# Optimization experiments

Hardware: AMD Instinct MI355X
Metric: run time of the kernel (lower is better)

## Reference

```python
import jax, jax.numpy as jnp
import numpy as np

B, S, H = 128, 512, 512

def _xavier(key, shape):
    fan_in, fan_out = shape[1], shape[0]
    limit = float(np.sqrt(6.0 / (fan_in + fan_out)))
    return jax.random.uniform(key, shape, jnp.float32, -limit, limit)

def setup_inputs() -> dict:
    key = jax.random.key(0)
    k1, k2, k3, k4, k5 = jax.random.split(key, 5)
    return {
        "h": jax.random.normal(k1, (B, S, H), jnp.float32),
        "x": jax.random.normal(k2, (B, S, H), jnp.float32),
        "Ve": _xavier(k3, (1, H)),
        "U1": _xavier(k4, (H, 2 * H)),
        "U2": _xavier(k5, (H, H)),
    }

def reference(h, x, Ve, U1, U2):
    # h: [B,S,H], x: [B,S,H]
    h_last = h[:, -1, :]                      # [B,H]
    U1a, U1b = U1[:, :U1.shape[0]], U1[:, U1.shape[0]:]  # each [H,H]
    # u1 = concat(h_t, h_last) @ U1.T, vectorized over t
    u1 = jnp.einsum('bsh,kh->bsk', h, U1a) + jnp.einsum('bh,kh->bk', h_last, U1b)[:, None, :]
    u2 = jnp.einsum('bsh,kh->bsk', x, U2)
    u = jnp.tanh(u1 + u2)                     # [B,S,H]
    e = jnp.einsum('bsk,k->bs', u, Ve[0])     # [B,S]
    alpha = jax.nn.softmax(e, axis=1)         # [B,S]
    context = jnp.einsum('bs,bsh->bh', alpha, h)
    return context
```

## Files before the change

kernel.cpp:

```cpp
#include <hip/hip_runtime.h>
#include <cstdint>
#include <cstddef>


typedef _Float16 h8 __attribute__((ext_vector_type(8)));
typedef float    f4 __attribute__((ext_vector_type(4)));

#define GLOAD16(g, l)                                                          \
  __builtin_amdgcn_global_load_lds(                                            \
      (const __attribute__((address_space(1))) void*)(g),                      \
      (__attribute__((address_space(3))) void*)(l), 16, 0, 0)

__device__ __forceinline__ float fast_tanh(float v) {
  float ex = __expf(2.0f * v);
  return 1.0f - 2.0f / (ex + 1.0f);
}

__global__ __launch_bounds__(256)
void cvt_kernel(const float* __restrict__ src, _Float16* __restrict__ dst, int n8) {
  const int stride = gridDim.x * 256;
  for (int i = blockIdx.x * 256 + threadIdx.x; i < n8; i += stride) {
    const float* p = src + (size_t)i * 8;
    f4 a = *(const f4*)p, b = *(const f4*)(p + 4);
    _Float16 hv[8];
    hv[0]=(_Float16)a[0]; hv[1]=(_Float16)a[1]; hv[2]=(_Float16)a[2]; hv[3]=(_Float16)a[3];
    hv[4]=(_Float16)b[0]; hv[5]=(_Float16)b[1]; hv[6]=(_Float16)b[2]; hv[7]=(_Float16)b[3];
    *(uint4*)(dst + (size_t)i * 8) = *(uint4*)hv;
  }
}

__global__ void bsetup2_kernel(const float* __restrict__ U1, const float* __restrict__ U2,
                               _Float16* __restrict__ Bimg) {
  int g = blockIdx.x * 256 + threadIdx.x;
  int l15 = g & 15;
  int grp = (g >> 4) & 7;
  int s   = (g >> 7) & 7;
  int kt  = (g >> 10) & 15;
  int nt  = g >> 14;
  int n = nt * 128 + grp * 16 + l15;
  int k = kt * 64 + s * 8;
  const float* p = (k < 512) ? (U1 + (size_t)n * 1024 + k)
                             : (U2 + (size_t)n * 512 + (k - 512));
  f4 a = *(const f4*)p, b = *(const f4*)(p + 4);
  _Float16 hv[8];
  hv[0]=(_Float16)a[0]; hv[1]=(_Float16)a[1]; hv[2]=(_Float16)a[2]; hv[3]=(_Float16)a[3];
  hv[4]=(_Float16)b[0]; hv[5]=(_Float16)b[1]; hv[6]=(_Float16)b[2]; hv[7]=(_Float16)b[3];
  *(uint4*)(Bimg + (size_t)g * 8) = *(uint4*)hv;
}

__global__ void bias_kernel(const float* __restrict__ hT, const float* __restrict__ U1,
                            float* __restrict__ bias) {
  const int b = blockIdx.x, t = threadIdx.x;
  const int l = t & 63, w = t >> 6;
  __shared__ float4 hl[128];
  if (t < 128) hl[t] = *(const float4*)(hT + ((size_t)b * 512 + 511) * 512 + t * 4);
  __syncthreads();
  for (int n = w; n < 512; n += 4) {
    const float4* ur = (const float4*)(U1 + (size_t)n * 1024 + 512);
    float4 u0 = ur[l],      u1 = ur[l + 64];
    float4 h0 = hl[l],      h1 = hl[l + 64];
    float s = u0.x*h0.x + u0.y*h0.y + u0.z*h0.z + u0.w*h0.w
            + u1.x*h1.x + u1.y*h1.y + u1.z*h1.z + u1.w*h1.w;
#pragma unroll
    for (int d = 1; d < 64; d <<= 1) s += __shfl_xor(s, d, 64);
    if (l == 0) bias[(size_t)b * 512 + n] = s;
  }
}

__global__ __launch_bounds__(256, 2)
void gemm3_kernel(const _Float16* __restrict__ hF, const _Float16* __restrict__ xF,
                  const _Float16* __restrict__ Bimg, const float* __restrict__ bias,
                  const float* __restrict__ Ve, float* __restrict__ e) {
  const int bid  = ((int)blockIdx.x & 7) * 256 + ((int)blockIdx.x >> 3);
  const int bm   = bid >> 2;
  const int nt   = bid & 3;
  const int row0 = bm * 128;
  const int bb   = row0 >> 9;
  const int t    = threadIdx.x;
  const int l    = t & 63;
  const int wv   = t >> 6;
  const int wm   = wv >> 1, wn = wv & 1;
  const int l15  = l & 15, lhi = l >> 4;

  __shared__ __align__(16) _Float16 Asm[2][8192];
  __shared__ __align__(16) _Float16 Bsm[2][8192];

  const int aoff0 = (wv * 32 + (l >> 3)) * 512 + (((l & 7) ^ (l >> 3)) << 3);

  auto STAGE = [&](int c, int kt) {
    const _Float16* ah = ((kt < 8) ? hF : xF) + (size_t)row0 * 512 + (kt & 7) * 64;
#pragma unroll
    for (int j = 0; j < 4; ++j)
      GLOAD16(ah + aoff0 + j * 4096, &Asm[c][wv * 2048 + j * 512]);
    const _Float16* bt = Bimg + ((size_t)(nt * 16 + kt) << 13);
#pragma unroll
    for (int j = 0; j < 4; ++j)
      GLOAD16(bt + wv * 2048 + j * 512 + l * 8, &Bsm[c][wv * 2048 + j * 512]);
  };

  const int vA0 = wm * 4096 + l15 * 64 + (((0 + lhi) ^ (l15 & 7)) << 3);
  const int vA1 = wm * 4096 + l15 * 64 + (((4 + lhi) ^ (l15 & 7)) << 3);
  const int vB  = lhi * 1024 + wn * 512 + l15 * 8;

  f4 acc[4][4];
#pragma unroll
  for (int mf = 0; mf < 4; ++mf)
#pragma unroll
    for (int nf = 0; nf < 4; ++nf)
      acc[mf][nf] = (f4){0.f, 0.f, 0.f, 0.f};

  STAGE(0, 0);
  STAGE(1, 1);
  asm volatile("s_waitcnt vmcnt(8)\n\ts_barrier" ::: "memory");
  __builtin_amdgcn_sched_barrier(0);

  for (int kt = 0; kt < 16; ++kt) {
    const int c = kt & 1;
#pragma unroll
    for (int kk = 0; kk < 2; ++kk) {
      h8 af[4], bf[4];
      const int a0 = (kk ? vA1 : vA0);
#pragma unroll
      for (int mf = 0; mf < 4; ++mf)
        af[mf] = *(const h8*)&Asm[c][a0 + mf * 1024];
#pragma unroll
      for (int nf = 0; nf < 4; ++nf)
        bf[nf] = *(const h8*)&Bsm[c][vB + kk * 4096 + nf * 128];
#pragma unroll
      for (int mf = 0; mf < 4; ++mf)
#pragma unroll
        for (int nf = 0; nf < 4; ++nf)
          acc[mf][nf] = __builtin_amdgcn_mfma_f32_16x16x32_f16(af[mf], bf[nf], acc[mf][nf], 0, 0, 0);
    }
    if (kt == 15) break;
    asm volatile("s_waitcnt lgkmcnt(0)\n\ts_barrier" ::: "memory");
    __builtin_amdgcn_sched_barrier(0);
    if (kt < 14) {
      STAGE(c, kt + 2);
      asm volatile("s_waitcnt vmcnt(8)\n\ts_barrier" ::: "memory");
    } else {
      asm volatile("s_waitcnt vmcnt(0)\n\ts_barrier" ::: "memory");
    }
    __builtin_amdgcn_sched_barrier(0);
  }

  float vev[4], biasv[4];
#pragma unroll
  for (int nf = 0; nf < 4; ++nf) {
    int c = nt * 128 + wn * 64 + nf * 16 + l15;
    vev[nf]   = Ve[c];
    biasv[nf] = bias[(size_t)bb * 512 + c];
  }
#pragma unroll
  for (int mf = 0; mf < 4; ++mf) {
#pragma unroll
    for (int j = 0; j < 4; ++j) {
      float s = 0.f;
#pragma unroll
      for (int nf = 0; nf < 4; ++nf)
        s += fast_tanh(acc[mf][nf][j] + biasv[nf]) * vev[nf];
#pragma unroll
      for (int m = 1; m < 16; m <<= 1) s += __shfl_xor(s, m, 64);
      if (l15 == 0) atomicAdd(&e[row0 + wm * 64 + mf * 16 + lhi * 4 + j], s);
    }
  }
}

__global__ __launch_bounds__(512)
void smax_ctx_kernel(const _Float16* __restrict__ hF, const float* __restrict__ e,
                     float* __restrict__ out) {
  const int b  = blockIdx.x >> 2;
  const int sc = blockIdx.x & 3;
  const int t  = threadIdx.x;
  __shared__ float al[512];
  __shared__ float redm[8], reds[8];
  float v = e[(size_t)b * 512 + t];
  float m = v;
#pragma unroll
  for (int d = 1; d < 64; d <<= 1) m = fmaxf(m, __shfl_xor(m, d, 64));
  if ((t & 63) == 0) redm[t >> 6] = m;
  __syncthreads();
  m = redm[0];
#pragma unroll
  for (int i = 1; i < 8; ++i) m = fmaxf(m, redm[i]);
  float ev = __expf(v - m);
  al[t] = ev;
  float s = ev;
#pragma unroll
  for (int d = 1; d < 64; d <<= 1) s += __shfl_xor(s, d, 64);
  if ((t & 63) == 0) reds[t >> 6] = s;
  __syncthreads();
  s = reds[0];
#pragma unroll
  for (int i = 1; i < 8; ++i) s += reds[i];
  const float inv = 1.0f / s;
  const _Float16* hp = hF + ((size_t)b * 512 + sc * 128) * 512 + t;
  float acc = 0.f;
#pragma unroll 4
  for (int q = 0; q < 128; ++q) acc += al[sc * 128 + q] * (float)hp[(size_t)q * 512];
  atomicAdd(&out[(size_t)b * 512 + t], acc * inv);
}

extern "C" void kernel_launch(void* const* d_in, const int* in_sizes, int n_in,
                              void* d_out, int out_size, void* d_ws, size_t ws_size,
                              hipStream_t stream) {
  const float* h  = (const float*)d_in[0];
  const float* x  = (const float*)d_in[1];
  const float* Ve = (const float*)d_in[2];
  const float* U1 = (const float*)d_in[3];
  const float* U2 = (const float*)d_in[4];
  float* out = (float*)d_out;

  const size_t MB = 1u << 20;
  if (ws_size < 130 * MB) return;

  _Float16* hF   = (_Float16*)d_ws;
  _Float16* xF   = (_Float16*)((char*)d_ws + 64 * MB);
  _Float16* Bimg = (_Float16*)((char*)d_ws + 128 * MB);
  float*    bias = (float*)((char*)d_ws + 129 * MB);
  float*    e    = (float*)((char*)d_ws + 129 * MB + 256 * 1024);

  hipMemsetAsync(e, 0, 65536 * sizeof(float), stream);
  hipMemsetAsync(d_out, 0, 65536 * sizeof(float), stream);

  cvt_kernel<<<4096, 256, 0, stream>>>(h, hF, 4194304);
  cvt_kernel<<<4096, 256, 0, stream>>>(x, xF, 4194304);
  bsetup2_kernel<<<256, 256, 0, stream>>>(U1, U2, Bimg);
  bias_kernel<<<128, 256, 0, stream>>>(h, U1, bias);
  gemm3_kernel<<<2048, 256, 0, stream>>>(hF, xF, Bimg, bias, Ve, e);
  smax_ctx_kernel<<<512, 512, 0, stream>>>(hF, e, out);
}
```

Measured before the change: 275.6 us.

## Use 8-wave GEMM blocks with smaller per-wave tiles and merge conversion kernels

The GEMM block grows from 4 to 8 waves (512 threads), and each wave now computes a 64x32 tile instead of 64x64, which halves its accumulator registers and raises occupancy. The B-operand image layout is changed to match the new wave split. The pipeline moves from a hand-tuned two-stage prefetch with explicit vmcnt waits to a simpler prefetch-next-stage scheme using __syncthreads. The two h/x fp16 conversion launches are merged into one kernel. The trade-off is less per-wave operand reuse and coarser synchronization, in exchange for more waves available to hide latency.

Measured after the change: 290.2 us. +5.3%, slower.

```diff
diff --git a/kernel.cpp b/kernel.cpp
--- a/kernel.cpp
+++ b/kernel.cpp
@@ -17,28 +17,33 @@
 }
 
 __global__ __launch_bounds__(256)
-void cvt_kernel(const float* __restrict__ src, _Float16* __restrict__ dst, int n8) {
+void cvt2_kernel(const float* __restrict__ h, const float* __restrict__ x,
+                 _Float16* __restrict__ hF, _Float16* __restrict__ xF) {
   const int stride = gridDim.x * 256;
-  for (int i = blockIdx.x * 256 + threadIdx.x; i < n8; i += stride) {
-    const float* p = src + (size_t)i * 8;
+  for (int i = blockIdx.x * 256 + threadIdx.x; i < 8388608; i += stride) {
+    const bool isH = i < 4194304;
+    const float* p = (isH ? h : x) + ((size_t)(i & 4194303)) * 8;
+    _Float16* d = (isH ? hF : xF) + ((size_t)(i & 4194303)) * 8;
     f4 a = *(const f4*)p, b = *(const f4*)(p + 4);
     _Float16 hv[8];
     hv[0]=(_Float16)a[0]; hv[1]=(_Float16)a[1]; hv[2]=(_Float16)a[2]; hv[3]=(_Float16)a[3];
     hv[4]=(_Float16)b[0]; hv[5]=(_Float16)b[1]; hv[6]=(_Float16)b[2]; hv[7]=(_Float16)b[3];
-    *(uint4*)(dst + (size_t)i * 8) = *(uint4*)hv;
-  }
-}
-
-__global__ void bsetup2_kernel(const float* __restrict__ U1, const float* __restrict__ U2,
+    *(uint4*)d = *(uint4*)hv;
+  }
+}
+
+__global__ void bsetup3_kernel(const float* __restrict__ U1, const float* __restrict__ U2,
                                _Float16* __restrict__ Bimg) {
   int g = blockIdx.x * 256 + threadIdx.x;
-  int l15 = g & 15;
-  int grp = (g >> 4) & 7;
-  int s   = (g >> 7) & 7;
+  int gt  = g & 1023;
   int kt  = (g >> 10) & 15;
   int nt  = g >> 14;
-  int n = nt * 128 + grp * 16 + l15;
-  int k = kt * 64 + s * 8;
+  int l15 = gt & 15;
+  int nf  = (gt >> 4) & 1;
+  int wn  = (gt >> 5) & 3;
+  int c8  = gt >> 7;
+  int n = nt * 128 + wn * 32 + nf * 16 + l15;
+  int k = kt * 64 + c8 * 8;
   const float* p = (k < 512) ? (U1 + (size_t)n * 1024 + k)
                              : (U2 + (size_t)n * 512 + (k - 512));
   f4 a = *(const f4*)p, b = *(const f4*)(p + 4);
@@ -67,8 +72,8 @@
   }
 }
 
-__global__ __launch_bounds__(256, 2)
-void gemm3_kernel(const _Float16* __restrict__ hF, const _Float16* __restrict__ xF,
+__global__ __launch_bounds__(512, 4)
+void gemm4_kernel(const _Float16* __restrict__ hF, const _Float16* __restrict__ xF,
                   const _Float16* __restrict__ Bimg, const float* __restrict__ bias,
                   const float* __restrict__ Ve, float* __restrict__ e) {
   const int bid  = ((int)blockIdx.x & 7) * 256 + ((int)blockIdx.x >> 3);
@@ -79,75 +84,63 @@
   const int t    = threadIdx.x;
   const int l    = t & 63;
   const int wv   = t >> 6;
-  const int wm   = wv >> 1, wn = wv & 1;
+  const int wm   = wv >> 2, wn = wv & 3;
   const int l15  = l & 15, lhi = l >> 4;
 
   __shared__ __align__(16) _Float16 Asm[2][8192];
   __shared__ __align__(16) _Float16 Bsm[2][8192];
 
-  const int aoff0 = (wv * 32 + (l >> 3)) * 512 + (((l & 7) ^ (l >> 3)) << 3);
+  const int aoff0 = (wv * 16 + (l >> 3)) * 512 + (((l & 7) ^ (l >> 3)) << 3);
 
   auto STAGE = [&](int c, int kt) {
     const _Float16* ah = ((kt < 8) ? hF : xF) + (size_t)row0 * 512 + (kt & 7) * 64;
-#pragma unroll
-    for (int j = 0; j < 4; ++j)
-      GLOAD16(ah + aoff0 + j * 4096, &Asm[c][wv * 2048 + j * 512]);
+    GLOAD16(ah + aoff0,        &Asm[c][wv * 1024]);
+    GLOAD16(ah + aoff0 + 4096, &Asm[c][wv * 1024 + 512]);
     const _Float16* bt = Bimg + ((size_t)(nt * 16 + kt) << 13);
-#pragma unroll
-    for (int j = 0; j < 4; ++j)
-      GLOAD16(bt + wv * 2048 + j * 512 + l * 8, &Bsm[c][wv * 2048 + j * 512]);
+    GLOAD16(bt + (wv * 128 + l) * 8,        &Bsm[c][wv * 1024]);
+    GLOAD16(bt + (wv * 128 + 64 + l) * 8,   &Bsm[c][wv * 1024 + 512]);
   };
 
-  const int vA0 = wm * 4096 + l15 * 64 + (((0 + lhi) ^ (l15 & 7)) << 3);
-  const int vA1 = wm * 4096 + l15 * 64 + (((4 + lhi) ^ (l15 & 7)) << 3);
-  const int vB  = lhi * 1024 + wn * 512 + l15 * 8;
-
-  f4 acc[4][4];
+  const int vA  = (wm * 64 + l15) * 64;
+  const int vB0 = wn * 256 + l15 * 8;
+
+  f4 acc[4][2];
 #pragma unroll
   for (int mf = 0; mf < 4; ++mf)
 #pragma unroll
-    for (int nf = 0; nf < 4; ++nf)
+    for (int nf = 0; nf < 2; ++nf)
       acc[mf][nf] = (f4){0.f, 0.f, 0.f, 0.f};
 
   STAGE(0, 0);
-  STAGE(1, 1);
-  asm volatile("s_waitcnt vmcnt(8)\n\ts_barrier" ::: "memory");
-  __builtin_amdgcn_sched_barrier(0);
+  __syncthreads();
 
   for (int kt = 0; kt < 16; ++kt) {
     const int c = kt & 1;
+    if (kt < 15) STAGE(c ^ 1, kt + 1);
 #pragma unroll
     for (int kk = 0; kk < 2; ++kk) {
-      h8 af[4], bf[4];
-      const int a0 = (kk ? vA1 : vA0);
+      const int c8 = kk * 4 + lhi;
+      const int aoffk = vA + ((c8 ^ (l15 & 7)) << 3);
+      h8 af[4], bf[2];
 #pragma unroll
       for (int mf = 0; mf < 4; ++mf)
-        af[mf] = *(const h8*)&Asm[c][a0 + mf * 1024];
-#pragma unroll
-      for (int nf = 0; nf < 4; ++nf)
-        bf[nf] = *(const h8*)&Bsm[c][vB + kk * 4096 + nf * 128];
+        af[mf] = *(const h8*)&Asm[c][aoffk + mf * 1024];
+#pragma unroll
+      for (int nf = 0; nf < 2; ++nf)
+        bf[nf] = *(const h8*)&Bsm[c][c8 * 1024 + vB0 + nf * 128];
 #pragma unroll
       for (int mf = 0; mf < 4; ++mf)
 #pragma unroll
-        for (int nf = 0; nf < 4; ++nf)
+        for (int nf = 0; nf < 2; ++nf)
           acc[mf][nf] = __builtin_amdgcn_mfma_f32_16x16x32_f16(af[mf], bf[nf], acc[mf][nf], 0, 0, 0);
     }
-    if (kt == 15) break;
-    asm volatile("s_waitcnt lgkmcnt(0)\n\ts_barrier" ::: "memory");
-    __builtin_amdgcn_sched_barrier(0);
-    if (kt < 14) {
-      STAGE(c, kt + 2);
-      asm volatile("s_waitcnt vmcnt(8)\n\ts_barrier" ::: "memory");
-    } else {
-      asm volatile("s_waitcnt vmcnt(0)\n\ts_barrier" ::: "memory");
-    }
-    __builtin_amdgcn_sched_barrier(0);
-  }
-
-  float vev[4], biasv[4];
-#pragma unroll
-  for (int nf = 0; nf < 4; ++nf) {
-    int c = nt * 128 + wn * 64 + nf * 16 + l15;
+    __syncthreads();
+  }
+
+  float vev[2], biasv[2];
+#pragma unroll
+  for (int nf = 0; nf < 2; ++nf) {
+    int c = nt * 128 + wn * 32 + nf * 16 + l15;
     vev[nf]   = Ve[c];
     biasv[nf] = bias[(size_t)bb * 512 + c];
   }
@@ -155,10 +148,8 @@
   for (int mf = 0; mf < 4; ++mf) {
 #pragma unroll
     for (int j = 0; j < 4; ++j) {
-      float s = 0.f;
-#pragma unroll
-      for (int nf = 0; nf < 4; ++nf)
-        s += fast_tanh(acc[mf][nf][j] + biasv[nf]) * vev[nf];
+      float s = fast_tanh(acc[mf][0][j] + biasv[0]) * vev[0]
+              + fast_tanh(acc[mf][1][j] + biasv[1]) * vev[1];
 #pragma unroll
       for (int m = 1; m < 16; m <<= 1) s += __shfl_xor(s, m, 64);
       if (l15 == 0) atomicAdd(&e[row0 + wm * 64 + mf * 16 + lhi * 4 + j], s);
@@ -223,10 +214,9 @@
   hipMemsetAsync(e, 0, 65536 * sizeof(float), stream);
   hipMemsetAsync(d_out, 0, 65536 * sizeof(float), stream);
 
-  cvt_kernel<<<4096, 256, 0, stream>>>(h, hF, 4194304);
-  cvt_kernel<<<4096, 256, 0, stream>>>(x, xF, 4194304);
-  bsetup2_kernel<<<256, 256, 0, stream>>>(U1, U2, Bimg);
+  cvt2_kernel<<<4096, 256, 0, stream>>>(h, x, hF, xF);
+  bsetup3_kernel<<<256, 256, 0, stream>>>(U1, U2, Bimg);
   bias_kernel<<<128, 256, 0, stream>>>(h, U1, bias);
-  gemm3_kernel<<<2048, 256, 0, stream>>>(hF, xF, Bimg, bias, Ve, e);
+  gemm4_kernel<<<2048, 512, 0, stream>>>(hF, xF, Bimg, bias, Ve, e);
   smax_ctx_kernel<<<512, 512, 0, stream>>>(hF, e, out);
 }
```

## Widen GEMM tile to 128x256 with 8 waves, triple-buffered LDS pipeline

Applied to the files above, without the earlier changes.

The GEMM now uses 512-thread blocks, each computing a 128x256 output tile. The pre-swizzled B image is re-laid out to match, so each block reads the A rows once per two column tiles instead of four. The LDS pipeline moves from double to triple buffering, with loads issued before compute so only one barrier is needed per k-step, and MFMA sections are raised in priority with s_setprio. The two conversion kernels are merged into one launch, and the bias kernel is reorganised so each wave keeps one U1 row in registers while looping over the batch. In exchange, the larger LDS footprint (144 KB per block) may limit occupancy.

Result: no change. 272.9 us (-1.0%).

```diff
diff --git a/kernel.cpp b/kernel.cpp
--- a/kernel.cpp
+++ b/kernel.cpp
@@ -17,28 +17,34 @@
 }
 
 __global__ __launch_bounds__(256)
-void cvt_kernel(const float* __restrict__ src, _Float16* __restrict__ dst, int n8) {
+void cvt2_kernel(const float* __restrict__ h, const float* __restrict__ x,
+                 _Float16* __restrict__ hF, _Float16* __restrict__ xF) {
   const int stride = gridDim.x * 256;
-  for (int i = blockIdx.x * 256 + threadIdx.x; i < n8; i += stride) {
-    const float* p = src + (size_t)i * 8;
+  for (int i = blockIdx.x * 256 + threadIdx.x; i < 8388608; i += stride) {
+    const bool isH = i < 4194304;
+    const float* p = (isH ? h : x) + ((size_t)(i & 4194303)) * 8;
+    _Float16* d = (isH ? hF : xF) + ((size_t)(i & 4194303)) * 8;
     f4 a = *(const f4*)p, b = *(const f4*)(p + 4);
     _Float16 hv[8];
     hv[0]=(_Float16)a[0]; hv[1]=(_Float16)a[1]; hv[2]=(_Float16)a[2]; hv[3]=(_Float16)a[3];
     hv[4]=(_Float16)b[0]; hv[5]=(_Float16)b[1]; hv[6]=(_Float16)b[2]; hv[7]=(_Float16)b[3];
-    *(uint4*)(dst + (size_t)i * 8) = *(uint4*)hv;
-  }
-}
-
-__global__ void bsetup2_kernel(const float* __restrict__ U1, const float* __restrict__ U2,
+    *(uint4*)d = *(uint4*)hv;
+  }
+}
+
+__global__ void bsetup4_kernel(const float* __restrict__ U1, const float* __restrict__ U2,
                                _Float16* __restrict__ Bimg) {
   int g = blockIdx.x * 256 + threadIdx.x;
-  int l15 = g & 15;
-  int grp = (g >> 4) & 7;
-  int s   = (g >> 7) & 7;
-  int kt  = (g >> 10) & 15;
-  int nt  = g >> 14;
-  int n = nt * 128 + grp * 16 + l15;
-  int k = kt * 64 + s * 8;
+  int c   = g & 2047;
+  int kt  = (g >> 11) & 15;
+  int nt  = g >> 15;
+  int l15 = c & 15;
+  int lhi = (c >> 4) & 3;
+  int kk  = (c >> 6) & 1;
+  int nf  = (c >> 7) & 3;
+  int wn  = c >> 9;
+  int n = nt * 256 + wn * 64 + nf * 16 + l15;
+  int k = kt * 64 + kk * 32 + lhi * 8;
   const float* p = (k < 512) ? (U1 + (size_t)n * 1024 + k)
                              : (U2 + (size_t)n * 512 + (k - 512));
   f4 a = *(const f4*)p, b = *(const f4*)(p + 4);
@@ -48,17 +54,17 @@
   *(uint4*)(Bimg + (size_t)g * 8) = *(uint4*)hv;
 }
 
-__global__ void bias_kernel(const float* __restrict__ hT, const float* __restrict__ U1,
-                            float* __restrict__ bias) {
-  const int b = blockIdx.x, t = threadIdx.x;
-  const int l = t & 63, w = t >> 6;
-  __shared__ float4 hl[128];
-  if (t < 128) hl[t] = *(const float4*)(hT + ((size_t)b * 512 + 511) * 512 + t * 4);
-  __syncthreads();
-  for (int n = w; n < 512; n += 4) {
-    const float4* ur = (const float4*)(U1 + (size_t)n * 1024 + 512);
-    float4 u0 = ur[l],      u1 = ur[l + 64];
-    float4 h0 = hl[l],      h1 = hl[l + 64];
+__global__ __launch_bounds__(256)
+void bias2_kernel(const float* __restrict__ hT, const float* __restrict__ U1,
+                  float* __restrict__ bias) {
+  const int t = threadIdx.x, l = t & 63, w = t >> 6;
+  const int n = blockIdx.x * 4 + w;
+  const float4* ur = (const float4*)(U1 + (size_t)n * 1024 + 512);
+  const float4 u0 = ur[l], u1 = ur[l + 64];
+#pragma unroll 4
+  for (int b = 0; b < 128; ++b) {
+    const float4* hp = (const float4*)(hT + ((size_t)b * 512 + 511) * 512);
+    float4 h0 = hp[l], h1 = hp[l + 64];
     float s = u0.x*h0.x + u0.y*h0.y + u0.z*h0.z + u0.w*h0.w
             + u1.x*h1.x + u1.y*h1.y + u1.z*h1.z + u1.w*h1.w;
 #pragma unroll
@@ -67,40 +73,44 @@
   }
 }
 
-__global__ __launch_bounds__(256, 2)
-void gemm3_kernel(const _Float16* __restrict__ hF, const _Float16* __restrict__ xF,
+__global__ __launch_bounds__(512, 2)
+void gemm5_kernel(const _Float16* __restrict__ hF, const _Float16* __restrict__ xF,
                   const _Float16* __restrict__ Bimg, const float* __restrict__ bias,
                   const float* __restrict__ Ve, float* __restrict__ e) {
-  const int bid  = ((int)blockIdx.x & 7) * 256 + ((int)blockIdx.x >> 3);
-  const int bm   = bid >> 2;
-  const int nt   = bid & 3;
+  const int bid  = ((int)blockIdx.x & 7) * 128 + ((int)blockIdx.x >> 3);
+  const int bm   = bid >> 1;
+  const int nt   = bid & 1;
   const int row0 = bm * 128;
   const int bb   = row0 >> 9;
   const int t    = threadIdx.x;
   const int l    = t & 63;
   const int wv   = t >> 6;
-  const int wm   = wv >> 1, wn = wv & 1;
+  const int wm   = wv >> 2, wn = wv & 3;
   const int l15  = l & 15, lhi = l >> 4;
 
-  __shared__ __align__(16) _Float16 Asm[2][8192];
-  __shared__ __align__(16) _Float16 Bsm[2][8192];
-
-  const int aoff0 = (wv * 32 + (l >> 3)) * 512 + (((l & 7) ^ (l >> 3)) << 3);
-
-  auto STAGE = [&](int c, int kt) {
+  __shared__ __align__(16) _Float16 Asm[3][8192];
+  __shared__ __align__(16) _Float16 Bsm[3][16384];
+
+  const int aoff0 = (wv * 16 + (l >> 3)) * 512 + (((l & 7) ^ (l >> 3)) << 3);
+
+  auto STAGE = [&](int buf, int kt) {
     const _Float16* ah = ((kt < 8) ? hF : xF) + (size_t)row0 * 512 + (kt & 7) * 64;
+    _Float16* Ad = &Asm[buf][wv * 1024];
+    GLOAD16(ah + aoff0,        Ad);
+    GLOAD16(ah + aoff0 + 4096, Ad + 512);
+    const _Float16* bt = Bimg + ((size_t)(nt * 16 + kt) << 14);
+    _Float16* Bd = &Bsm[buf][wv * 512];
 #pragma unroll
     for (int j = 0; j < 4; ++j)
-      GLOAD16(ah + aoff0 + j * 4096, &Asm[c][wv * 2048 + j * 512]);
-    const _Float16* bt = Bimg + ((size_t)(nt * 16 + kt) << 13);
-#pragma unroll
-    for (int j = 0; j < 4; ++j)
-      GLOAD16(bt + wv * 2048 + j * 512 + l * 8, &Bsm[c][wv * 2048 + j * 512]);
+      GLOAD16(bt + j * 4096 + wv * 512 + l * 8, Bd + j * 4096);
   };
 
-  const int vA0 = wm * 4096 + l15 * 64 + (((0 + lhi) ^ (l15 & 7)) << 3);
-  const int vA1 = wm * 4096 + l15 * 64 + (((4 + lhi) ^ (l15 & 7)) << 3);
-  const int vB  = lhi * 1024 + wn * 512 + l15 * 8;
+  const int aBase = (wm * 64 + l15) * 64;
+  const int b2  = (l15 >> 2) & 1;
+  const int lo2 = lhi ^ (l15 & 3);
+  const int ak0 = ((((0 ^ b2) << 2) | lo2) << 3);
+  const int ak1 = ((((1 ^ b2) << 2) | lo2) << 3);
+  const int bBase = wn * 4096 + l * 8;
 
   f4 acc[4][4];
 #pragma unroll
@@ -111,43 +121,49 @@
 
   STAGE(0, 0);
   STAGE(1, 1);
-  asm volatile("s_waitcnt vmcnt(8)\n\ts_barrier" ::: "memory");
+  asm volatile("s_waitcnt vmcnt(6)\n\ts_barrier" ::: "memory");
   __builtin_amdgcn_sched_barrier(0);
 
+  int bc = 0;
   for (int kt = 0; kt < 16; ++kt) {
-    const int c = kt & 1;
+    if (kt < 14) {
+      int bp = bc + 2; if (bp >= 3) bp -= 3;
+      STAGE(bp, kt + 2);
+    }
+    const _Float16* Ab = &Asm[bc][0];
+    const _Float16* Bb = &Bsm[bc][0];
 #pragma unroll
     for (int kk = 0; kk < 2; ++kk) {
       h8 af[4], bf[4];
-      const int a0 = (kk ? vA1 : vA0);
+      const int akk = kk ? ak1 : ak0;
 #pragma unroll
       for (int mf = 0; mf < 4; ++mf)
-        af[mf] = *(const h8*)&Asm[c][a0 + mf * 1024];
+        af[mf] = *(const h8*)&Ab[aBase + mf * 1024 + akk];
 #pragma unroll
       for (int nf = 0; nf < 4; ++nf)
-        bf[nf] = *(const h8*)&Bsm[c][vB + kk * 4096 + nf * 128];
+        bf[nf] = *(const h8*)&Bb[bBase + nf * 1024 + kk * 512];
+      __builtin_amdgcn_s_setprio(1);
 #pragma unroll
       for (int mf = 0; mf < 4; ++mf)
 #pragma unroll
         for (int nf = 0; nf < 4; ++nf)
           acc[mf][nf] = __builtin_amdgcn_mfma_f32_16x16x32_f16(af[mf], bf[nf], acc[mf][nf], 0, 0, 0);
-    }
-    if (kt == 15) break;
-    asm volatile("s_waitcnt lgkmcnt(0)\n\ts_barrier" ::: "memory");
-    __builtin_amdgcn_sched_barrier(0);
+      __builtin_amdgcn_s_setprio(0);
+    }
     if (kt < 14) {
-      STAGE(c, kt + 2);
-      asm volatile("s_waitcnt vmcnt(8)\n\ts_barrier" ::: "memory");
-    } else {
+      asm volatile("s_waitcnt vmcnt(6)\n\ts_barrier" ::: "memory");
+      __builtin_amdgcn_sched_barrier(0);
+    } else if (kt == 14) {
       asm volatile("s_waitcnt vmcnt(0)\n\ts_barrier" ::: "memory");
-    }
-    __builtin_amdgcn_sched_barrier(0);
+      __builtin_amdgcn_sched_barrier(0);
+    }
+    bc = bc + 1; if (bc == 3) bc = 0;
   }
 
   float vev[4], biasv[4];
 #pragma unroll
   for (int nf = 0; nf < 4; ++nf) {
-    int c = nt * 128 + wn * 64 + nf * 16 + l15;
+    int c = nt * 256 + wn * 64 + nf * 16 + l15;
     vev[nf]   = Ve[c];
     biasv[nf] = bias[(size_t)bb * 512 + c];
   }
@@ -223,10 +239,9 @@
   hipMemsetAsync(e, 0, 65536 * sizeof(float), stream);
   hipMemsetAsync(d_out, 0, 65536 * sizeof(float), stream);
 
-  cvt_kernel<<<4096, 256, 0, stream>>>(h, hF, 4194304);
-  cvt_kernel<<<4096, 256, 0, stream>>>(x, xF, 4194304);
-  bsetup2_kernel<<<256, 256, 0, stream>>>(U1, U2, Bimg);
-  bias_kernel<<<128, 256, 0, stream>>>(h, U1, bias);
-  gemm3_kernel<<<2048, 256, 0, stream>>>(hF, xF, Bimg, bias, Ve, e);
+  cvt2_kernel<<<4096, 256, 0, stream>>>(h, x, hF, xF);
+  bsetup4_kernel<<<256, 256, 0, stream>>>(U1, U2, Bimg);
+  bias2_kernel<<<128, 256, 0, stream>>>(h, U1, bias);
+  gemm5_kernel<<<1024, 512, 0, stream>>>(hF, xF, Bimg, bias, Ve, e);
   smax_ctx_kernel<<<512, 512, 0, stream>>>(hF, e, out);
 }
```
